# Kernel tuning notes

Measured on AMD Instinct MI355X. Metric: run time of the kernel, lower is better.

The kernel has to match this reference:

```python
import jax, jax.numpy as jnp
import numpy as np

BLANK_LOGPROB = -1.0
NEG = -1e30  # finite stand-in for -inf (safe in fp32/bf16, differentiable masking)


def setup_inputs() -> dict:
    key = jax.random.key(0)
    k1, k2, k3 = jax.random.split(key, 3)
    B, T, L = 64, 2000, 400
    attn_logprob = jax.random.normal(k1, (B, 1, T, L), dtype=jnp.float32)
    # guarantee mel_len >= 2*text_len + 1 so the CTC path is always feasible
    text_lens = jax.random.randint(k2, (B,), 100, L + 1, dtype=jnp.int32)
    mel_lens = jax.random.randint(k3, (B,), 1000, T + 1, dtype=jnp.int32)
    return {"attn_logprob": attn_logprob, "text_lens": text_lens, "mel_lens": mel_lens}


def reference(attn_logprob, text_lens, mel_lens):
    B, _, T, L = attn_logprob.shape
    x = attn_logprob[:, 0]                                            # [B, T, L]
    # pad a blank class at index 0 along the text dim (pad=(1,0) in torch)
    x = jnp.pad(x, ((0, 0), (0, 0), (1, 0)), constant_values=BLANK_LOGPROB)
    # NOTE: the original log-softmaxes the FULL (unsliced) padded tensor
    lp = jax.nn.log_softmax(x, axis=-1)                               # [B, T, L+1]

    # CTC with targets = [1..text_len] (all distinct), blank = 0.
    # Extended label sequence: blank, 1, blank, 2, ..., blank, L, blank -> S = 2L+1
    S = 2 * L + 1
    s = jnp.arange(S)
    lab = jnp.where(s % 2 == 0, 0, s // 2 + 1)                        # [S] class id per ext pos
    is_label = (s % 2 == 1)                                           # skip transition allowed (no repeats)
    valid = s[None, :] < (2 * text_lens[:, None] + 1)                 # [B, S]

    neg = jnp.asarray(NEG, lp.dtype)
    emit = jnp.take(lp, lab, axis=2)                                  # [B, T, S]
    emit = jnp.where(valid[:, None, :], emit, neg)
    emits = jnp.swapaxes(emit, 0, 1)                                  # [T, B, S]

    alpha0 = jnp.where(s[None, :] < 2, emits[0], neg)                 # [B, S]

    def shift(a, k):
        return jnp.concatenate([jnp.full((B, k), neg, a.dtype), a[:, :S - k]], axis=1)

    def step(alpha, xs):
        e_t, t = xs
        stacked = jnp.stack(
            [alpha,
             shift(alpha, 1),
             jnp.where(is_label[None, :], shift(alpha, 2), neg)], axis=0)
        new = e_t + jax.scipy.special.logsumexp(stacked, axis=0)
        # freeze alpha once past this sample's input length
        new = jnp.where((t < mel_lens)[:, None], new, alpha)
        return new, None

    alpha, _ = jax.lax.scan(step, alpha0, (emits[1:], jnp.arange(1, T)))

    end = jnp.stack([2 * text_lens, 2 * text_lens - 1], axis=1)       # [B, 2]
    a_end = jnp.take_along_axis(alpha, end, axis=1)
    logalpha = jax.scipy.special.logsumexp(a_end, axis=1)             # [B]
    # torch CTCLoss(reduction='mean') divides each sample by target_length;
    # the module then averages over batch. zero_infinity -> zero out infinite losses.
    loss = -logalpha / text_lens.astype(lp.dtype)
    loss = jnp.where(logalpha > NEG / 2, loss, jnp.zeros_like(loss))
    return jnp.mean(loss)
```

## Files before the change

kernel.cpp:

```cpp
#include <hip/hip_runtime.h>
#include <math.h>


namespace {
constexpr int kB = 64;
constexpr int kT = 2000;
constexpr int kL = 400;
constexpr int kC = 16;
constexpr int kRow = 408;
constexpr float kEblank = 0.36787944117144233f;
}

__global__ __launch_bounds__(256, 1) void ctc_forward_kernel(
        const float* __restrict__ attn, const int* __restrict__ text_lens,
        const int* __restrict__ mel_lens, float* __restrict__ loss_ws) {
    __shared__ __align__(16) float wbuf[2][kC][kRow];
    __shared__ float psum[2][kC * 100];
    __shared__ double sLd;

    const int b    = blockIdx.x;
    const int tid  = threadIdx.x;
    const int lane = tid & 63;
    const int wv   = tid >> 6;
    const int Lb = text_lens[b];
    const int Tb = mel_lens[b];
    const int Sb = 2 * Lb + 1;
    const int nck = (Tb + kC - 1) / kC;

    const float4* __restrict__ rp4 = (const float4*)(attn + (size_t)b * kT * kL);

    {
        const int slot = tid >> 7, row = (tid >> 3) & 15, j = tid & 7;
        wbuf[slot][row][400 + j] = 0.f;
    }

    const int pid = tid - 64;
    float4 rgE[9], rgO[9];

    auto load_chunk = [&](int ck, float4 (&rg)[9]) {
        const int t0 = ck * kC;
        #pragma unroll
        for (int i = 0; i < 9; ++i) {
            const int task = pid + 192 * i;
            if (task < kC * 100) {
                const int r = task / 100, q = task - r * 100;
                if (t0 + r < Tb) rg[i] = rp4[(size_t)(t0 + r) * 100 + q];
            }
        }
    };
    auto store_chunk = [&](int ck, const float4 (&rg)[9]) {
        const int slot = ck & 1;
        const int t0 = ck * kC;
        #pragma unroll
        for (int i = 0; i < 9; ++i) {
            const int task = pid + 192 * i;
            if (task < kC * 100) {
                const int r = task / 100, q = task - r * 100;
                float s4 = 0.f;
                if (t0 + r < Tb) {
                    const float4 x = rg[i];
                    const float e0 = __expf(x.x), e1 = __expf(x.y);
                    const float e2 = __expf(x.z), e3 = __expf(x.w);
                    s4 = (e0 + e1) + (e2 + e3);
                    const int l0 = 4 * q;
                    float4 w4;
                    w4.x = (l0 + 0 < Lb) ? e0 : 0.f;
                    w4.y = (l0 + 1 < Lb) ? e1 : 0.f;
                    w4.z = (l0 + 2 < Lb) ? e2 : 0.f;
                    w4.w = (l0 + 3 < Lb) ? e3 : 0.f;
                    *(float4*)&wbuf[slot][r][4 * q] = w4;
                }
                psum[slot][task] = s4;
            }
        }
    };

    double Ld = 0.0;
    auto reduce_lse = [&](int ck) {
        const int ps = ck & 1;
        const int r = lane >> 2, k = lane & 3;
        float s = 0.f;
        #pragma unroll
        for (int m = 0; m < 25; ++m) s += psum[ps][r * 100 + k + 4 * m];
        s += __shfl_xor(s, 1);
        s += __shfl_xor(s, 2);
        float lv = (k == 0 && (ck * kC + r) < Tb) ? __logf(s + kEblank) : 0.f;
        lv += __shfl_xor(lv, 4);
        lv += __shfl_xor(lv, 8);
        lv += __shfl_xor(lv, 16);
        lv += __shfl_xor(lv, 32);
        Ld += (double)lv;
    };

    const int gi  = (lane < 50) ? lane : 50;
    float a[16];
    #pragma unroll
    for (int i = 0; i < 16; ++i) a[i] = 0.f;
    double Ct = 0.0;
    float red = 1.0f;

    auto shift1 = [&](float x) -> float {
        return __int_as_float(__builtin_amdgcn_update_dpp(
            0, __float_as_int(x), 0x138, 0xf, 0xf, true));
    };

    auto step = [&](const float* __restrict__ wr) {
        float w[8];
        *(float4*)&w[0] = *(const float4*)(wr);
        *(float4*)&w[4] = *(const float4*)(wr + 4);
        const float p1 = shift1(a[15]);
        float n[16];
        {
            const float s = a[0] + p1;
            n[0] = kEblank * s;
            n[1] = w[0] * (a[1] + s);
        }
        #pragma unroll
        for (int j = 1; j < 8; ++j) {
            const float s = a[2 * j] + a[2 * j - 1];
            n[2 * j]     = kEblank * s;
            n[2 * j + 1] = w[j] * (a[2 * j + 1] + s);
        }
        #pragma unroll
        for (int i = 0; i < 16; ++i) a[i] = n[i];
    };
    auto fold = [&]() {
        const float tot = red;
        const float c = 1.0f / tot;
        Ct += (double)__logf(tot);
        float ns = 0.f;
        #pragma unroll
        for (int i = 0; i < 16; ++i) { a[i] *= c; ns += a[i]; }
        red = ns;
    };
    auto consumer_chunk = [&](int ck) {
        const float* wr = &wbuf[ck & 1][0][8 * gi];
        if (ck == 0) {
            if (lane == 0) { a[0] = kEblank; a[1] = wbuf[0][0][0]; }
            #pragma unroll
            for (int r = 1; r < kC; ++r) step(wr + r * kRow);
            fold();
        } else if (ck < nck - 1) {
            step(wr);             red += __shfl_xor(red, 1);
            step(wr + kRow);      red += __shfl_xor(red, 2);
            step(wr + 2 * kRow);  red += __shfl_xor(red, 4);
            step(wr + 3 * kRow);  red += __shfl_xor(red, 8);
            step(wr + 4 * kRow);  red += __shfl_xor(red, 16);
            step(wr + 5 * kRow);  red += __shfl_xor(red, 32);
            #pragma unroll
            for (int r = 6; r < kC; ++r) step(wr + r * kRow);
            fold();
        } else {
            const int t0 = ck * kC;
            for (int r = 0; r < kC; ++r) {
                if (t0 + r >= Tb) break;
                step(wr + r * kRow);
            }
        }
    };

    if (wv > 0) {
        load_chunk(0, rgE);
        store_chunk(0, rgE);
        load_chunk(1, rgO);
    }
    __syncthreads();

    for (int ck = 0; ck < nck; ck += 2) {
        if (wv == 0) {
            consumer_chunk(ck);
        } else {
            if (ck + 1 < nck) store_chunk(ck + 1, rgO);
            load_chunk(ck + 2, rgE);
            if (wv == 1) reduce_lse(ck);
        }
        __syncthreads();
        if (ck + 1 < nck) {
            if (wv == 0) {
                consumer_chunk(ck + 1);
            } else {
                if (ck + 2 < nck) store_chunk(ck + 2, rgE);
                load_chunk(ck + 3, rgO);
                if (wv == 1) reduce_lse(ck + 1);
            }
            __syncthreads();
        }
    }

    float* afin = (float*)wbuf;
    if (wv == 0 && lane <= 50) {
        #pragma unroll
        for (int i = 0; i < 16; ++i) afin[16 * lane + i] = a[i];
    }
    if (wv == 1 && lane == 0) sLd = Ld;
    __syncthreads();
    if (tid == 0) {
        const float tail = afin[Sb - 2] + afin[Sb - 1];
        const double la = (double)__logf(tail) + Ct - sLd;
        float loss = 0.f;
        if (la > -5e29) loss = (float)(-la / (double)Lb);
        loss_ws[b] = loss;
    }
}

__global__ void mean64_kernel(const float* __restrict__ loss_ws,
                              float* __restrict__ out) {
    float v = loss_ws[threadIdx.x];
    #pragma unroll
    for (int off = 32; off > 0; off >>= 1) v += __shfl_xor(v, off);
    if (threadIdx.x == 0) out[0] = v * (1.0f / 64.0f);
}

extern "C" void kernel_launch(void* const* d_in, const int* in_sizes, int n_in,
                              void* d_out, int out_size, void* d_ws, size_t ws_size,
                              hipStream_t stream) {
    const float* attn      = (const float*)d_in[0];
    const int*   text_lens = (const int*)d_in[1];
    const int*   mel_lens  = (const int*)d_in[2];
    float* loss_ws = (float*)d_ws;

    ctc_forward_kernel<<<kB, 256, 0, stream>>>(attn, text_lens, mel_lens, loss_ws);
    mean64_kernel<<<1, 64, 0, stream>>>(loss_ws, (float*)d_out);
}
```

Baseline: 541.8 us.

## Halve chunk size and preload LDS emission rows into registers before recurrence

Cuts the time chunk from 16 to 8 rows, which shrinks producer register arrays and the LDS buffers and changes the log-sum-exp reduction lane mapping to match. The consumer wave now loads all eight rows of emission weights from LDS up front, so the serial recurrence steps run on registers without waiting on LDS. The trade-off is a barrier every 8 timesteps instead of 16, twice as many chunk-level syncs and folds, and higher register pressure in the consumer from the preloaded rows.

```diff
diff --git a/kernel.cpp b/kernel.cpp
--- a/kernel.cpp
+++ b/kernel.cpp
@@ -6,7 +6,7 @@
 constexpr int kB = 64;
 constexpr int kT = 2000;
 constexpr int kL = 400;
-constexpr int kC = 16;
+constexpr int kC = 8;
 constexpr int kRow = 408;
 constexpr float kEblank = 0.36787944117144233f;
 }
@@ -29,18 +29,18 @@
 
     const float4* __restrict__ rp4 = (const float4*)(attn + (size_t)b * kT * kL);
 
-    {
-        const int slot = tid >> 7, row = (tid >> 3) & 15, j = tid & 7;
+    if (tid < 128) {
+        const int slot = tid >> 6, row = (tid >> 3) & 7, j = tid & 7;
         wbuf[slot][row][400 + j] = 0.f;
     }
 
     const int pid = tid - 64;
-    float4 rgE[9], rgO[9];
-
-    auto load_chunk = [&](int ck, float4 (&rg)[9]) {
+    float4 rgE[5], rgO[5];
+
+    auto load_chunk = [&](int ck, float4 (&rg)[5]) {
         const int t0 = ck * kC;
         #pragma unroll
-        for (int i = 0; i < 9; ++i) {
+        for (int i = 0; i < 5; ++i) {
             const int task = pid + 192 * i;
             if (task < kC * 100) {
                 const int r = task / 100, q = task - r * 100;
@@ -48,11 +48,11 @@
             }
         }
     };
-    auto store_chunk = [&](int ck, const float4 (&rg)[9]) {
+    auto store_chunk = [&](int ck, const float4 (&rg)[5]) {
         const int slot = ck & 1;
         const int t0 = ck * kC;
         #pragma unroll
-        for (int i = 0; i < 9; ++i) {
+        for (int i = 0; i < 5; ++i) {
             const int task = pid + 192 * i;
             if (task < kC * 100) {
                 const int r = task / 100, q = task - r * 100;
@@ -78,14 +78,17 @@
     double Ld = 0.0;
     auto reduce_lse = [&](int ck) {
         const int ps = ck & 1;
-        const int r = lane >> 2, k = lane & 3;
+        const int r = lane >> 3, k = lane & 7;
         float s = 0.f;
         #pragma unroll
-        for (int m = 0; m < 25; ++m) s += psum[ps][r * 100 + k + 4 * m];
+        for (int m = 0; m < 13; ++m) {
+            const int q = k + 8 * m;
+            if (q < 100) s += psum[ps][r * 100 + q];
+        }
         s += __shfl_xor(s, 1);
         s += __shfl_xor(s, 2);
+        s += __shfl_xor(s, 4);
         float lv = (k == 0 && (ck * kC + r) < Tb) ? __logf(s + kEblank) : 0.f;
-        lv += __shfl_xor(lv, 4);
         lv += __shfl_xor(lv, 8);
         lv += __shfl_xor(lv, 16);
         lv += __shfl_xor(lv, 32);
@@ -104,11 +107,11 @@
             0, __float_as_int(x), 0x138, 0xf, 0xf, true));
     };
 
-    auto step = [&](const float* __restrict__ wr) {
+    auto step_reg = [&](const float4 wlo, const float4 whi) {
+        const float p1 = shift1(a[15]);
         float w[8];
-        *(float4*)&w[0] = *(const float4*)(wr);
-        *(float4*)&w[4] = *(const float4*)(wr + 4);
-        const float p1 = shift1(a[15]);
+        w[0] = wlo.x; w[1] = wlo.y; w[2] = wlo.z; w[3] = wlo.w;
+        w[4] = whi.x; w[5] = whi.y; w[6] = whi.z; w[7] = whi.w;
         float n[16];
         {
             const float s = a[0] + p1;
@@ -124,6 +127,11 @@
         #pragma unroll
         for (int i = 0; i < 16; ++i) a[i] = n[i];
     };
+    auto step_mem = [&](const float* __restrict__ wr_row) {
+        const float4 wlo = *(const float4*)(wr_row);
+        const float4 whi = *(const float4*)(wr_row + 4);
+        step_reg(wlo, whi);
+    };
     auto fold = [&]() {
         const float tot = red;
         const float c = 1.0f / tot;
@@ -133,31 +141,46 @@
         for (int i = 0; i < 16; ++i) { a[i] *= c; ns += a[i]; }
         red = ns;
     };
+
+#define PRELOAD(R)                                                      \
+    const float4 WA##R = *(const float4*)(wr + (R) * kRow);             \
+    const float4 WB##R = *(const float4*)(wr + (R) * kRow + 4);
+
     auto consumer_chunk = [&](int ck) {
         const float* wr = &wbuf[ck & 1][0][8 * gi];
         if (ck == 0) {
+            PRELOAD(1) PRELOAD(2) PRELOAD(3) PRELOAD(4)
+            PRELOAD(5) PRELOAD(6) PRELOAD(7)
             if (lane == 0) { a[0] = kEblank; a[1] = wbuf[0][0][0]; }
-            #pragma unroll
-            for (int r = 1; r < kC; ++r) step(wr + r * kRow);
+            step_reg(WA1, WB1);
+            step_reg(WA2, WB2);
+            step_reg(WA3, WB3);
+            step_reg(WA4, WB4);
+            step_reg(WA5, WB5);
+            step_reg(WA6, WB6);
+            step_reg(WA7, WB7);
             fold();
         } else if (ck < nck - 1) {
-            step(wr);             red += __shfl_xor(red, 1);
-            step(wr + kRow);      red += __shfl_xor(red, 2);
-            step(wr + 2 * kRow);  red += __shfl_xor(red, 4);
-            step(wr + 3 * kRow);  red += __shfl_xor(red, 8);
-            step(wr + 4 * kRow);  red += __shfl_xor(red, 16);
-            step(wr + 5 * kRow);  red += __shfl_xor(red, 32);
-            #pragma unroll
-            for (int r = 6; r < kC; ++r) step(wr + r * kRow);
+            PRELOAD(0) PRELOAD(1) PRELOAD(2) PRELOAD(3)
+            PRELOAD(4) PRELOAD(5) PRELOAD(6) PRELOAD(7)
+            step_reg(WA0, WB0);  red += __shfl_xor(red, 1);
+            step_reg(WA1, WB1);  red += __shfl_xor(red, 2);
+            step_reg(WA2, WB2);  red += __shfl_xor(red, 4);
+            step_reg(WA3, WB3);  red += __shfl_xor(red, 8);
+            step_reg(WA4, WB4);  red += __shfl_xor(red, 16);
+            step_reg(WA5, WB5);  red += __shfl_xor(red, 32);
+            step_reg(WA6, WB6);
+            step_reg(WA7, WB7);
             fold();
         } else {
             const int t0 = ck * kC;
             for (int r = 0; r < kC; ++r) {
                 if (t0 + r >= Tb) break;
-                step(wr + r * kRow);
-            }
-        }
-    };
+                step_mem(wr + r * kRow);
+            }
+        }
+    };
+#undef PRELOAD
 
     if (wv > 0) {
         load_chunk(0, rgE);
```

Measured after the change: 869.0 us. 1.6x slower.

## Collapse producer/consumer warps into one wave with register-prefetched rows

Applied to the files above, without the earlier changes.

Replaces the four-wave producer/consumer design, which staged exp-weights through double-buffered LDS with block barriers, with a single 64-lane wave per sample. That wave loads its own 8 labels per timestep into registers 16 steps ahead, computes the exps and the wave-wide softmax denominator inline, and runs a reformulated recurrence over combined blank+label state (u/o). This removes the LDS round trips and __syncthreads per chunk. In exchange, the exp, denominator reduction and global loads now sit on the serial critical path of the recurrence, and each block has only one wave.

```diff
diff --git a/kernel.cpp b/kernel.cpp
--- a/kernel.cpp
+++ b/kernel.cpp
@@ -6,201 +6,190 @@
 constexpr int kB = 64;
 constexpr int kT = 2000;
 constexpr int kL = 400;
-constexpr int kC = 16;
-constexpr int kRow = 408;
 constexpr float kEblank = 0.36787944117144233f;
 }
 
-__global__ __launch_bounds__(256, 1) void ctc_forward_kernel(
+__device__ __forceinline__ float shift1(float x) {
+    return __int_as_float(__builtin_amdgcn_update_dpp(
+        0, __float_as_int(x), 0x138, 0xf, 0xf, true));
+}
+
+__device__ __forceinline__ float wave_sum(float x) {
+    x += __shfl_xor(x, 1);
+    x += __shfl_xor(x, 2);
+    x += __shfl_xor(x, 4);
+    x += __shfl_xor(x, 8);
+    x += __shfl_xor(x, 16);
+    x += __shfl_xor(x, 32);
+    return x;
+}
+
+__global__ __launch_bounds__(64, 1) void ctc_forward_kernel(
         const float* __restrict__ attn, const int* __restrict__ text_lens,
         const int* __restrict__ mel_lens, float* __restrict__ loss_ws) {
-    __shared__ __align__(16) float wbuf[2][kC][kRow];
-    __shared__ float psum[2][kC * 100];
-    __shared__ double sLd;
+    __shared__ float su[512];
 
     const int b    = blockIdx.x;
-    const int tid  = threadIdx.x;
-    const int lane = tid & 63;
-    const int wv   = tid >> 6;
+    const int lane = threadIdx.x;
     const int Lb = text_lens[b];
     const int Tb = mel_lens[b];
-    const int Sb = 2 * Lb + 1;
-    const int nck = (Tb + kC - 1) / kC;
-
-    const float4* __restrict__ rp4 = (const float4*)(attn + (size_t)b * kT * kL);
-
-    {
-        const int slot = tid >> 7, row = (tid >> 3) & 15, j = tid & 7;
-        wbuf[slot][row][400 + j] = 0.f;
-    }
-
-    const int pid = tid - 64;
-    float4 rgE[9], rgO[9];
-
-    auto load_chunk = [&](int ck, float4 (&rg)[9]) {
-        const int t0 = ck * kC;
+    const int nck = (Tb + 15) / 16;
+
+    const bool ldok = lane < 50;
+    const int  l0   = 8 * lane;
+    const int  qa   = 2 * lane;
+    const float4* __restrict__ rp4 =
+        (const float4*)(attn + (size_t)b * kT * kL);
+
+    float4 A[8][2], Bk[8][2];
+    #pragma unroll
+    for (int r = 0; r < 8; ++r) {
+        A[r][0] = A[r][1] = Bk[r][0] = Bk[r][1] = make_float4(0.f, 0.f, 0.f, 0.f);
+    }
+
+    float u[8], o[8];
+    #pragma unroll
+    for (int i = 0; i < 8; ++i) { u[i] = 0.f; o[i] = 0.f; }
+    double Ct = 0.0;
+    double Ld = 0.0;
+    float  ldc = 0.f;
+
+#define LOADSLOT(BK, r, t)                                               \
+    if (ldok && (t) < Tb) {                                              \
+        BK[r][0] = rp4[(t) * 100 + qa];                                  \
+        BK[r][1] = rp4[(t) * 100 + qa + 1];                              \
+    }
+
+#define DENOM(XA, XB)                                                    \
+    const float e0 = __expf((XA).x), e1 = __expf((XA).y);                \
+    const float e2 = __expf((XA).z), e3 = __expf((XA).w);                \
+    const float e4 = __expf((XB).x), e5 = __expf((XB).y);                \
+    const float e6 = __expf((XB).z), e7 = __expf((XB).w);                \
+    {                                                                    \
+        const float s8 = ((e0 + e1) + (e2 + e3)) + ((e4 + e5) + (e6 + e7)); \
+        ldc += __logf(wave_sum(ldok ? s8 : 0.f) + kEblank);              \
+    }
+
+#define RECUR()                                                          \
+    {                                                                    \
+        const float w0 = (l0 + 0 < Lb) ? e0 : 0.f;                       \
+        const float w1 = (l0 + 1 < Lb) ? e1 : 0.f;                       \
+        const float w2 = (l0 + 2 < Lb) ? e2 : 0.f;                       \
+        const float w3 = (l0 + 3 < Lb) ? e3 : 0.f;                       \
+        const float w4 = (l0 + 4 < Lb) ? e4 : 0.f;                       \
+        const float w5 = (l0 + 5 < Lb) ? e5 : 0.f;                       \
+        const float w6 = (l0 + 6 < Lb) ? e6 : 0.f;                       \
+        const float w7 = (l0 + 7 < Lb) ? e7 : 0.f;                       \
+        const float op7 = w7 * (o[7] + u[7]);                            \
+        const float p   = shift1(op7);                                   \
+        const float op0 = w0 * (o[0] + u[0]);                            \
+        const float op1 = w1 * (o[1] + u[1]);                            \
+        const float op2 = w2 * (o[2] + u[2]);                            \
+        const float op3 = w3 * (o[3] + u[3]);                            \
+        const float op4 = w4 * (o[4] + u[4]);                            \
+        const float op5 = w5 * (o[5] + u[5]);                            \
+        const float op6 = w6 * (o[6] + u[6]);                            \
+        u[7] = __builtin_fmaf(kEblank, u[7], op6);                       \
+        u[6] = __builtin_fmaf(kEblank, u[6], op5);                       \
+        u[5] = __builtin_fmaf(kEblank, u[5], op4);                       \
+        u[4] = __builtin_fmaf(kEblank, u[4], op3);                       \
+        u[3] = __builtin_fmaf(kEblank, u[3], op2);                       \
+        u[2] = __builtin_fmaf(kEblank, u[2], op1);                       \
+        u[1] = __builtin_fmaf(kEblank, u[1], op0);                       \
+        u[0] = __builtin_fmaf(kEblank, u[0], p);                         \
+        o[0] = op0; o[1] = op1; o[2] = op2; o[3] = op3;                  \
+        o[4] = op4; o[5] = op5; o[6] = op6; o[7] = op7;                  \
+    }
+
+#define FULLSTEP(BK, r, t)                                               \
+    {                                                                    \
+        const float4 xa = BK[r][0], xb = BK[r][1];                       \
+        LOADSLOT(BK, r, (t) + 16)                                        \
+        DENOM(xa, xb)                                                    \
+        RECUR()                                                          \
+    }
+
+#define TAILSTEP(BK, r, t)                                               \
+    if ((t) < Tb) {                                                      \
+        const float4 xa = BK[r][0], xb = BK[r][1];                       \
+        DENOM(xa, xb)                                                    \
+        RECUR()                                                          \
+    }
+
+    auto fold = [&]() {
+        float ns = 0.f;
         #pragma unroll
-        for (int i = 0; i < 9; ++i) {
-            const int task = pid + 192 * i;
-            if (task < kC * 100) {
-                const int r = task / 100, q = task - r * 100;
-                if (t0 + r < Tb) rg[i] = rp4[(size_t)(t0 + r) * 100 + q];
-            }
-        }
-    };
-    auto store_chunk = [&](int ck, const float4 (&rg)[9]) {
-        const int slot = ck & 1;
-        const int t0 = ck * kC;
-        #pragma unroll
-        for (int i = 0; i < 9; ++i) {
-            const int task = pid + 192 * i;
-            if (task < kC * 100) {
-                const int r = task / 100, q = task - r * 100;
-                float s4 = 0.f;
-                if (t0 + r < Tb) {
-                    const float4 x = rg[i];
-                    const float e0 = __expf(x.x), e1 = __expf(x.y);
-                    const float e2 = __expf(x.z), e3 = __expf(x.w);
-                    s4 = (e0 + e1) + (e2 + e3);
-                    const int l0 = 4 * q;
-                    float4 w4;
-                    w4.x = (l0 + 0 < Lb) ? e0 : 0.f;
-                    w4.y = (l0 + 1 < Lb) ? e1 : 0.f;
-                    w4.z = (l0 + 2 < Lb) ? e2 : 0.f;
-                    w4.w = (l0 + 3 < Lb) ? e3 : 0.f;
-                    *(float4*)&wbuf[slot][r][4 * q] = w4;
-                }
-                psum[slot][task] = s4;
-            }
-        }
-    };
-
-    double Ld = 0.0;
-    auto reduce_lse = [&](int ck) {
-        const int ps = ck & 1;
-        const int r = lane >> 2, k = lane & 3;
-        float s = 0.f;
-        #pragma unroll
-        for (int m = 0; m < 25; ++m) s += psum[ps][r * 100 + k + 4 * m];
-        s += __shfl_xor(s, 1);
-        s += __shfl_xor(s, 2);
-        float lv = (k == 0 && (ck * kC + r) < Tb) ? __logf(s + kEblank) : 0.f;
-        lv += __shfl_xor(lv, 4);
-        lv += __shfl_xor(lv, 8);
-        lv += __shfl_xor(lv, 16);
-        lv += __shfl_xor(lv, 32);
-        Ld += (double)lv;
-    };
-
-    const int gi  = (lane < 50) ? lane : 50;
-    float a[16];
-    #pragma unroll
-    for (int i = 0; i < 16; ++i) a[i] = 0.f;
-    double Ct = 0.0;
-    float red = 1.0f;
-
-    auto shift1 = [&](float x) -> float {
-        return __int_as_float(__builtin_amdgcn_update_dpp(
-            0, __float_as_int(x), 0x138, 0xf, 0xf, true));
-    };
-
-    auto step = [&](const float* __restrict__ wr) {
-        float w[8];
-        *(float4*)&w[0] = *(const float4*)(wr);
-        *(float4*)&w[4] = *(const float4*)(wr + 4);
-        const float p1 = shift1(a[15]);
-        float n[16];
-        {
-            const float s = a[0] + p1;
-            n[0] = kEblank * s;
-            n[1] = w[0] * (a[1] + s);
-        }
-        #pragma unroll
-        for (int j = 1; j < 8; ++j) {
-            const float s = a[2 * j] + a[2 * j - 1];
-            n[2 * j]     = kEblank * s;
-            n[2 * j + 1] = w[j] * (a[2 * j + 1] + s);
-        }
-        #pragma unroll
-        for (int i = 0; i < 16; ++i) a[i] = n[i];
-    };
-    auto fold = [&]() {
-        const float tot = red;
+        for (int i = 0; i < 8; ++i) ns += u[i] + o[i];
+        const float tot = wave_sum(ns);
         const float c = 1.0f / tot;
         Ct += (double)__logf(tot);
-        float ns = 0.f;
+        Ld += (double)ldc;  ldc = 0.f;
         #pragma unroll
-        for (int i = 0; i < 16; ++i) { a[i] *= c; ns += a[i]; }
-        red = ns;
+        for (int i = 0; i < 8; ++i) { u[i] *= c; o[i] *= c; }
     };
-    auto consumer_chunk = [&](int ck) {
-        const float* wr = &wbuf[ck & 1][0][8 * gi];
-        if (ck == 0) {
-            if (lane == 0) { a[0] = kEblank; a[1] = wbuf[0][0][0]; }
-            #pragma unroll
-            for (int r = 1; r < kC; ++r) step(wr + r * kRow);
-            fold();
-        } else if (ck < nck - 1) {
-            step(wr);             red += __shfl_xor(red, 1);
-            step(wr + kRow);      red += __shfl_xor(red, 2);
-            step(wr + 2 * kRow);  red += __shfl_xor(red, 4);
-            step(wr + 3 * kRow);  red += __shfl_xor(red, 8);
-            step(wr + 4 * kRow);  red += __shfl_xor(red, 16);
-            step(wr + 5 * kRow);  red += __shfl_xor(red, 32);
-            #pragma unroll
-            for (int r = 6; r < kC; ++r) step(wr + r * kRow);
-            fold();
-        } else {
-            const int t0 = ck * kC;
-            for (int r = 0; r < kC; ++r) {
-                if (t0 + r >= Tb) break;
-                step(wr + r * kRow);
-            }
+
+    #pragma unroll
+    for (int r = 0; r < 8; ++r) { LOADSLOT(A,  r, r) }
+    #pragma unroll
+    for (int r = 0; r < 8; ++r) { LOADSLOT(Bk, r, 8 + r) }
+
+    {
+        {
+            const float4 xa = A[0][0], xb = A[0][1];
+            LOADSLOT(A, 0, 16)
+            DENOM(xa, xb)
+            if (lane == 0) { u[0] = kEblank; o[0] = e0; }
         }
-    };
-
-    if (wv > 0) {
-        load_chunk(0, rgE);
-        store_chunk(0, rgE);
-        load_chunk(1, rgO);
-    }
+        FULLSTEP(A, 1, 1)  FULLSTEP(A, 2, 2)  FULLSTEP(A, 3, 3)
+        FULLSTEP(A, 4, 4)  FULLSTEP(A, 5, 5)  FULLSTEP(A, 6, 6)
+        FULLSTEP(A, 7, 7)
+        FULLSTEP(Bk, 0, 8)  FULLSTEP(Bk, 1, 9)  FULLSTEP(Bk, 2, 10)
+        FULLSTEP(Bk, 3, 11) FULLSTEP(Bk, 4, 12) FULLSTEP(Bk, 5, 13)
+        FULLSTEP(Bk, 6, 14) FULLSTEP(Bk, 7, 15)
+        fold();
+    }
+
+    for (int ck = 1; ck < nck - 1; ++ck) {
+        const int t0 = ck * 16;
+        FULLSTEP(A, 0, t0 + 0)  FULLSTEP(A, 1, t0 + 1)
+        FULLSTEP(A, 2, t0 + 2)  FULLSTEP(A, 3, t0 + 3)
+        FULLSTEP(A, 4, t0 + 4)  FULLSTEP(A, 5, t0 + 5)
+        FULLSTEP(A, 6, t0 + 6)  FULLSTEP(A, 7, t0 + 7)
+        FULLSTEP(Bk, 0, t0 + 8)  FULLSTEP(Bk, 1, t0 + 9)
+        FULLSTEP(Bk, 2, t0 + 10) FULLSTEP(Bk, 3, t0 + 11)
+        FULLSTEP(Bk, 4, t0 + 12) FULLSTEP(Bk, 5, t0 + 13)
+        FULLSTEP(Bk, 6, t0 + 14) FULLSTEP(Bk, 7, t0 + 15)
+        fold();
+    }
+
+    {
+        const int t0 = (nck - 1) * 16;
+        TAILSTEP(A, 0, t0 + 0)  TAILSTEP(A, 1, t0 + 1)
+        TAILSTEP(A, 2, t0 + 2)  TAILSTEP(A, 3, t0 + 3)
+        TAILSTEP(A, 4, t0 + 4)  TAILSTEP(A, 5, t0 + 5)
+        TAILSTEP(A, 6, t0 + 6)  TAILSTEP(A, 7, t0 + 7)
+        TAILSTEP(Bk, 0, t0 + 8)  TAILSTEP(Bk, 1, t0 + 9)
+        TAILSTEP(Bk, 2, t0 + 10) TAILSTEP(Bk, 3, t0 + 11)
+        TAILSTEP(Bk, 4, t0 + 12) TAILSTEP(Bk, 5, t0 + 13)
+        TAILSTEP(Bk, 6, t0 + 14) TAILSTEP(Bk, 7, t0 + 15)
+    }
+
+    #pragma unroll
+    for (int i = 0; i < 8; ++i) su[l0 + i] = u[i];
     __syncthreads();
-
-    for (int ck = 0; ck < nck; ck += 2) {
-        if (wv == 0) {
-            consumer_chunk(ck);
-        } else {
-            if (ck + 1 < nck) store_chunk(ck + 1, rgO);
-            load_chunk(ck + 2, rgE);
-            if (wv == 1) reduce_lse(ck);
-        }
-        __syncthreads();
-        if (ck + 1 < nck) {
-            if (wv == 0) {
-                consumer_chunk(ck + 1);
-            } else {
-                if (ck + 2 < nck) store_chunk(ck + 2, rgE);
-                load_chunk(ck + 3, rgO);
-                if (wv == 1) reduce_lse(ck + 1);
-            }
-            __syncthreads();
-        }
-    }
-
-    float* afin = (float*)wbuf;
-    if (wv == 0 && lane <= 50) {
-        #pragma unroll
-        for (int i = 0; i < 16; ++i) afin[16 * lane + i] = a[i];
-    }
-    if (wv == 1 && lane == 0) sLd = Ld;
-    __syncthreads();
-    if (tid == 0) {
-        const float tail = afin[Sb - 2] + afin[Sb - 1];
-        const double la = (double)__logf(tail) + Ct - sLd;
+    if (lane == 0) {
+        const float tail = su[Lb];
+        const double la = (double)__logf(tail) + Ct - Ld;
         float loss = 0.f;
         if (la > -5e29) loss = (float)(-la / (double)Lb);
         loss_ws[b] = loss;
     }
+
+#undef LOADSLOT
+#undef DENOM
+#undef RECUR
+#undef FULLSTEP
+#undef TAILSTEP
 }
 
 __global__ void mean64_kernel(const float* __restrict__ loss_ws,
@@ -219,6 +208,6 @@
     const int*   mel_lens  = (const int*)d_in[2];
     float* loss_ws = (float*)d_ws;
 
-    ctc_forward_kernel<<<kB, 256, 0, stream>>>(attn, text_lens, mel_lens, loss_ws);
+    ctc_forward_kernel<<<kB, 64, 0, stream>>>(attn, text_lens, mel_lens, loss_ws);
     mean64_kernel<<<1, 64, 0, stream>>>(loss_ws, (float*)d_out);
 }
```

New measurement: 846.1 us. 56.2% more time.

## Replace block barriers with LDS flag handshakes between consumer and producer waves

Applied to the files above, without the earlier changes.

Drops the per-chunk __syncthreads between the single consumer wave running the CTC recurrence and the three producer waves. Synchronisation now uses shared-memory counters: producers set per-slot ready flags and the consumer sets per-slot done counters, so each side waits only on its own dependency. Work is also remapped so each producer wave handles whole rows, computing the row log-sum-exp directly with a wave reduction, which removes the psum buffer and the separate reduction pass. The cost is spin-waiting with s_sleep and a dependence on correct LDS memory ordering via volatile accesses and lgkmcnt waits.

```diff
diff --git a/kernel.cpp b/kernel.cpp
--- a/kernel.cpp
+++ b/kernel.cpp
@@ -11,12 +11,25 @@
 constexpr float kEblank = 0.36787944117144233f;
 }
 
+__device__ __forceinline__ float shift1(float x) {
+    return __int_as_float(__builtin_amdgcn_update_dpp(
+        0, __float_as_int(x), 0x138, 0xf, 0xf, true));
+}
+
+__device__ __forceinline__ float wave_sum(float x) {
+    x += __shfl_xor(x, 1);  x += __shfl_xor(x, 2);
+    x += __shfl_xor(x, 4);  x += __shfl_xor(x, 8);
+    x += __shfl_xor(x, 16); x += __shfl_xor(x, 32);
+    return x;
+}
+
 __global__ __launch_bounds__(256, 1) void ctc_forward_kernel(
         const float* __restrict__ attn, const int* __restrict__ text_lens,
         const int* __restrict__ mel_lens, float* __restrict__ loss_ws) {
     __shared__ __align__(16) float wbuf[2][kC][kRow];
-    __shared__ float psum[2][kC * 100];
-    __shared__ double sLd;
+    __shared__ int prodflag[2][4];
+    __shared__ int conscnt[2];
+    __shared__ double sLdArr[4];
 
     const int b    = blockIdx.x;
     const int tid  = threadIdx.x;
@@ -29,174 +42,204 @@
 
     const float4* __restrict__ rp4 = (const float4*)(attn + (size_t)b * kT * kL);
 
+    if (tid < 8) prodflag[tid >> 2][tid & 3] = 0;
+    if (tid < 2) conscnt[tid] = 0;
     {
         const int slot = tid >> 7, row = (tid >> 3) & 15, j = tid & 7;
         wbuf[slot][row][400 + j] = 0.f;
     }
-
-    const int pid = tid - 64;
-    float4 rgE[9], rgO[9];
-
-    auto load_chunk = [&](int ck, float4 (&rg)[9]) {
-        const int t0 = ck * kC;
+    __syncthreads();
+
+    if (wv == 0) {
+        const int gi = (lane < 50) ? lane : 50;
+        float a[16];
         #pragma unroll
-        for (int i = 0; i < 9; ++i) {
-            const int task = pid + 192 * i;
-            if (task < kC * 100) {
-                const int r = task / 100, q = task - r * 100;
-                if (t0 + r < Tb) rg[i] = rp4[(size_t)(t0 + r) * 100 + q];
-            }
-        }
-    };
-    auto store_chunk = [&](int ck, const float4 (&rg)[9]) {
-        const int slot = ck & 1;
-        const int t0 = ck * kC;
+        for (int i = 0; i < 16; ++i) a[i] = 0.f;
+        double Ct = 0.0;
+        float red = 1.0f;
+
+        auto wait_ready = [&](int ck) {
+            const int s = ck & 1, tgt = (ck >> 1) + 1;
+            volatile int* p1 = &prodflag[s][1];
+            volatile int* p2 = &prodflag[s][2];
+            volatile int* p3 = &prodflag[s][3];
+            while (*p1 < tgt || *p2 < tgt || *p3 < tgt)
+                __builtin_amdgcn_s_sleep(1);
+            asm volatile("" ::: "memory");
+        };
+        auto signal_done = [&](int ck) {
+            const int s = ck & 1;
+            asm volatile("s_waitcnt lgkmcnt(0)" ::: "memory");
+            if (lane == 0) *(volatile int*)&conscnt[s] = (ck >> 1) + 1;
+        };
+
+        auto step = [&](const float* __restrict__ wr) {
+            float w[8];
+            *(float4*)&w[0] = *(const float4*)(wr);
+            *(float4*)&w[4] = *(const float4*)(wr + 4);
+            const float p1 = shift1(a[15]);
+            float n[16];
+            {
+                const float s = a[0] + p1;
+                n[0] = kEblank * s;
+                n[1] = w[0] * (a[1] + s);
+            }
+            #pragma unroll
+            for (int j = 1; j < 8; ++j) {
+                const float s = a[2 * j] + a[2 * j - 1];
+                n[2 * j]     = kEblank * s;
+                n[2 * j + 1] = w[j] * (a[2 * j + 1] + s);
+            }
+            #pragma unroll
+            for (int i = 0; i < 16; ++i) a[i] = n[i];
+        };
+        auto fold = [&]() {
+            const float tot = red;
+            const float c = 1.0f / tot;
+            Ct += (double)__logf(tot);
+            float ns = 0.f;
+            #pragma unroll
+            for (int i = 0; i < 16; ++i) { a[i] *= c; ns += a[i]; }
+            red = ns;
+        };
+
+        for (int ck = 0; ck < nck; ++ck) {
+            wait_ready(ck);
+            const float* wr = &wbuf[ck & 1][0][8 * gi];
+            if (ck == 0) {
+                if (lane == 0) { a[0] = kEblank; a[1] = wbuf[0][0][0]; }
+                #pragma unroll
+                for (int r = 1; r < kC; ++r) step(wr + r * kRow);
+                fold();
+            } else if (ck < nck - 1) {
+                step(wr);             red += __shfl_xor(red, 1);
+                step(wr + kRow);      red += __shfl_xor(red, 2);
+                step(wr + 2 * kRow);  red += __shfl_xor(red, 4);
+                step(wr + 3 * kRow);  red += __shfl_xor(red, 8);
+                step(wr + 4 * kRow);  red += __shfl_xor(red, 16);
+                step(wr + 5 * kRow);  red += __shfl_xor(red, 32);
+                #pragma unroll
+                for (int r = 6; r < kC; ++r) step(wr + r * kRow);
+                fold();
+            } else {
+                const int t0 = ck * kC;
+                for (int r = 0; r < kC; ++r) {
+                    if (t0 + r >= Tb) break;
+                    step(wr + r * kRow);
+                }
+            }
+            signal_done(ck);
+        }
+
+        float* afin = (float*)wbuf;
+        if (lane <= 50) {
+            #pragma unroll
+            for (int i = 0; i < 16; ++i) afin[16 * lane + i] = a[i];
+        }
+        if (lane == 0) sLdArr[0] = Ct;
+    } else {
+        const bool hi = (lane < 36);
+        double Ld = 0.0;
+        float4 pE[6][2], pO[6][2];
         #pragma unroll
-        for (int i = 0; i < 9; ++i) {
-            const int task = pid + 192 * i;
-            if (task < kC * 100) {
-                const int r = task / 100, q = task - r * 100;
-                float s4 = 0.f;
-                if (t0 + r < Tb) {
-                    const float4 x = rg[i];
-                    const float e0 = __expf(x.x), e1 = __expf(x.y);
-                    const float e2 = __expf(x.z), e3 = __expf(x.w);
-                    s4 = (e0 + e1) + (e2 + e3);
-                    const int l0 = 4 * q;
-                    float4 w4;
-                    w4.x = (l0 + 0 < Lb) ? e0 : 0.f;
-                    w4.y = (l0 + 1 < Lb) ? e1 : 0.f;
-                    w4.z = (l0 + 2 < Lb) ? e2 : 0.f;
-                    w4.w = (l0 + 3 < Lb) ? e3 : 0.f;
-                    *(float4*)&wbuf[slot][r][4 * q] = w4;
+        for (int i = 0; i < 6; ++i) {
+            pE[i][0] = pE[i][1] = pO[i][0] = pO[i][1] =
+                make_float4(0.f, 0.f, 0.f, 0.f);
+        }
+
+        auto wait_write_ok = [&](int ck) {
+            const int g = ck >> 1;
+            if (g == 0) return;
+            const int s = ck & 1;
+            volatile int* p = &conscnt[s];
+            while (*p < g) __builtin_amdgcn_s_sleep(2);
+            asm volatile("" ::: "memory");
+        };
+        auto signal_staged = [&](int ck) {
+            const int s = ck & 1;
+            asm volatile("s_waitcnt lgkmcnt(0)" ::: "memory");
+            if (lane == 0) *(volatile int*)&prodflag[s][wv] = (ck >> 1) + 1;
+        };
+
+        auto load_chunk = [&](int ck, float4 (&bank)[6][2]) {
+            const int t0 = ck * kC;
+            #pragma unroll
+            for (int i = 0; i < 6; ++i) {
+                const int r = (wv - 1) + 3 * i;
+                if (r < kC) {
+                    const int t = t0 + r;
+                    if (t < Tb) {
+                        bank[i][0] = rp4[(size_t)t * 100 + lane];
+                        if (hi) bank[i][1] = rp4[(size_t)t * 100 + 64 + lane];
+                    }
                 }
-                psum[slot][task] = s4;
-            }
-        }
-    };
-
-    double Ld = 0.0;
-    auto reduce_lse = [&](int ck) {
-        const int ps = ck & 1;
-        const int r = lane >> 2, k = lane & 3;
-        float s = 0.f;
-        #pragma unroll
-        for (int m = 0; m < 25; ++m) s += psum[ps][r * 100 + k + 4 * m];
-        s += __shfl_xor(s, 1);
-        s += __shfl_xor(s, 2);
-        float lv = (k == 0 && (ck * kC + r) < Tb) ? __logf(s + kEblank) : 0.f;
-        lv += __shfl_xor(lv, 4);
-        lv += __shfl_xor(lv, 8);
-        lv += __shfl_xor(lv, 16);
-        lv += __shfl_xor(lv, 32);
-        Ld += (double)lv;
-    };
-
-    const int gi  = (lane < 50) ? lane : 50;
-    float a[16];
-    #pragma unroll
-    for (int i = 0; i < 16; ++i) a[i] = 0.f;
-    double Ct = 0.0;
-    float red = 1.0f;
-
-    auto shift1 = [&](float x) -> float {
-        return __int_as_float(__builtin_amdgcn_update_dpp(
-            0, __float_as_int(x), 0x138, 0xf, 0xf, true));
-    };
-
-    auto step = [&](const float* __restrict__ wr) {
-        float w[8];
-        *(float4*)&w[0] = *(const float4*)(wr);
-        *(float4*)&w[4] = *(const float4*)(wr + 4);
-        const float p1 = shift1(a[15]);
-        float n[16];
-        {
-            const float s = a[0] + p1;
-            n[0] = kEblank * s;
-            n[1] = w[0] * (a[1] + s);
-        }
-        #pragma unroll
-        for (int j = 1; j < 8; ++j) {
-            const float s = a[2 * j] + a[2 * j - 1];
-            n[2 * j]     = kEblank * s;
-            n[2 * j + 1] = w[j] * (a[2 * j + 1] + s);
-        }
-        #pragma unroll
-        for (int i = 0; i < 16; ++i) a[i] = n[i];
-    };
-    auto fold = [&]() {
-        const float tot = red;
-        const float c = 1.0f / tot;
-        Ct += (double)__logf(tot);
-        float ns = 0.f;
-        #pragma unroll
-        for (int i = 0; i < 16; ++i) { a[i] *= c; ns += a[i]; }
-        red = ns;
-    };
-    auto consumer_chunk = [&](int ck) {
-        const float* wr = &wbuf[ck & 1][0][8 * gi];
-        if (ck == 0) {
-            if (lane == 0) { a[0] = kEblank; a[1] = wbuf[0][0][0]; }
-            #pragma unroll
-            for (int r = 1; r < kC; ++r) step(wr + r * kRow);
-            fold();
-        } else if (ck < nck - 1) {
-            step(wr);             red += __shfl_xor(red, 1);
-            step(wr + kRow);      red += __shfl_xor(red, 2);
-            step(wr + 2 * kRow);  red += __shfl_xor(red, 4);
-            step(wr + 3 * kRow);  red += __shfl_xor(red, 8);
-            step(wr + 4 * kRow);  red += __shfl_xor(red, 16);
-            step(wr + 5 * kRow);  red += __shfl_xor(red, 32);
-            #pragma unroll
-            for (int r = 6; r < kC; ++r) step(wr + r * kRow);
-            fold();
-        } else {
-            const int t0 = ck * kC;
-            for (int r = 0; r < kC; ++r) {
-                if (t0 + r >= Tb) break;
-                step(wr + r * kRow);
-            }
-        }
-    };
-
-    if (wv > 0) {
-        load_chunk(0, rgE);
-        store_chunk(0, rgE);
-        load_chunk(1, rgO);
+            }
+        };
+        auto store_chunk = [&](int ck, const float4 (&bank)[6][2]) {
+            const int slot = ck & 1, t0 = ck * kC;
+            float ldacc = 0.f;
+            #pragma unroll
+            for (int i = 0; i < 6; ++i) {
+                const int r = (wv - 1) + 3 * i;
+                if (r < kC) {
+                    const int t = t0 + r;
+                    if (t < Tb) {
+                        const float4 x0 = bank[i][0];
+                        const float e0 = __expf(x0.x), e1 = __expf(x0.y);
+                        const float e2 = __expf(x0.z), e3 = __expf(x0.w);
+                        float s = (e0 + e1) + (e2 + e3);
+                        const int l0 = 4 * lane;
+                        float4 w4;
+                        w4.x = (l0 + 0 < Lb) ? e0 : 0.f;
+                        w4.y = (l0 + 1 < Lb) ? e1 : 0.f;
+                        w4.z = (l0 + 2 < Lb) ? e2 : 0.f;
+                        w4.w = (l0 + 3 < Lb) ? e3 : 0.f;
+                        *(float4*)&wbuf[slot][r][l0] = w4;
+                        if (hi) {
+                            const float4 x1 = bank[i][1];
+                            const float e4 = __expf(x1.x), e5 = __expf(x1.y);
+                            const float e6 = __expf(x1.z), e7 = __expf(x1.w);
+                            s += (e4 + e5) + (e6 + e7);
+                            const int m0 = 256 + 4 * lane;
+                            float4 v4;
+                            v4.x = (m0 + 0 < Lb) ? e4 : 0.f;
+                            v4.y = (m0 + 1 < Lb) ? e5 : 0.f;
+                            v4.z = (m0 + 2 < Lb) ? e6 : 0.f;
+                            v4.w = (m0 + 3 < Lb) ? e7 : 0.f;
+                            *(float4*)&wbuf[slot][r][m0] = v4;
+                        }
+                        ldacc += __logf(wave_sum(s) + kEblank);
+                    }
+                }
+            }
+            Ld += (double)ldacc;
+        };
+
+        load_chunk(0, pE);
+        store_chunk(0, pE);
+        signal_staged(0);
+        load_chunk(1, pO);
+        for (int ck = 1; ck < nck; ck += 2) {
+            load_chunk(ck + 1, pE);
+            wait_write_ok(ck);
+            store_chunk(ck, pO);
+            signal_staged(ck);
+            if (ck + 1 < nck) {
+                load_chunk(ck + 2, pO);
+                wait_write_ok(ck + 1);
+                store_chunk(ck + 1, pE);
+                signal_staged(ck + 1);
+            }
+        }
+        if (lane == 0) sLdArr[wv] = Ld;
     }
-    __syncthreads();
-
-    for (int ck = 0; ck < nck; ck += 2) {
-        if (wv == 0) {
-            consumer_chunk(ck);
-        } else {
-            if (ck + 1 < nck) store_chunk(ck + 1, rgO);
-            load_chunk(ck + 2, rgE);
-            if (wv == 1) reduce_lse(ck);
-        }
-        __syncthreads();
-        if (ck + 1 < nck) {
-            if (wv == 0) {
-                consumer_chunk(ck + 1);
-            } else {
-                if (ck + 2 < nck) store_chunk(ck + 2, rgE);
-                load_chunk(ck + 3, rgO);
-                if (wv == 1) reduce_lse(ck + 1);
-            }
-            __syncthreads();
-        }
-    }
-
-    float* afin = (float*)wbuf;
-    if (wv == 0 && lane <= 50) {
-        #pragma unroll
-        for (int i = 0; i < 16; ++i) afin[16 * lane + i] = a[i];
-    }
-    if (wv == 1 && lane == 0) sLd = Ld;
+
     __syncthreads();
     if (tid == 0) {
+        const float* afin = (const float*)wbuf;
         const float tail = afin[Sb - 2] + afin[Sb - 1];
-        const double la = (double)__logf(tail) + Ct - sLd;
+        const double la = (double)__logf(tail) + sLdArr[0]
+                          - (sLdArr[1] + sLdArr[2] + sLdArr[3]);
         float loss = 0.f;
         if (la > -5e29) loss = (float)(-la / (double)Lb);
         loss_ws[b] = loss;
```

Result: slower. 599.4 us (+10.6%).
